# Kernel tuning notes

Measured on AMD Instinct MI355X. Metric: run time of the kernel, lower is better.

## Reference

```python
import jax, jax.numpy as jnp
from jax import lax
import numpy as np

N_NEURON = 4096
BATCH = 64
N_STEP = 200


def setup_inputs() -> dict:
    key = jax.random.key(0)
    k1, k2, k3 = jax.random.split(key, 3)
    # state_g is a sigmoid output: keep strictly inside (0, 1) for g_inverse's log
    state_g = jax.random.uniform(k1, (BATCH, N_NEURON), dtype=jnp.float32,
                                 minval=0.05, maxval=0.95)
    # Symmetric_Linear init: W ~ N(0, 0.01), symmetrized, zero diagonal
    W = jax.random.normal(k2, (N_NEURON, N_NEURON), dtype=jnp.float32) * 0.01
    W = W + W.T
    W = W - jnp.diag(jnp.diag(W))
    b = jax.random.normal(k3, (N_NEURON,), dtype=jnp.float32) * 0.01
    beta = jnp.ones((N_NEURON,), dtype=jnp.float32) * 10.0
    tau = jnp.ones((N_NEURON,), dtype=jnp.float32)
    dt_train = jnp.float32(0.1)
    return {"state_g": state_g, "W": W, "b": b, "beta": beta, "tau": tau,
            "dt_train": dt_train, "n_step": N_STEP}


def reference(state_g, W, b, beta, tau, dt_train, n_step):
    # max_x = 50 / beta.max()  (original uses .item(); beta is constant so same value)
    max_x = 50.0 / jnp.max(beta)
    # Symmetric_Linear effective weight: (W + W^T)/2 with zero diagonal.
    # Original recomputes this every step; it's step-invariant so hoist it.
    W_sym = (W + W.T) * 0.5 - jnp.diag(jnp.diag(W))
    # g_inverse: x = (1/beta) * log(g / (1 - g))
    state_x = (1.0 / beta) * jnp.log(state_g / (1.0 - state_g))
    alpha = dt_train / tau  # [N]

    def step(carry, _):
        x, g = carry
        pre = g @ W_sym.T + b                       # [B, N] GEMM
        x = alpha * pre + (1.0 - alpha) * x         # leaky update
        x = jnp.clip(x, -max_x, max_x)
        g = jax.nn.sigmoid(beta * x)
        return (x, g), None

    (state_x, state_g), _ = lax.scan(step, (state_x, state_g), None, length=n_step)
    return state_g
```

## Files before the change

kernel.cpp:

```cpp
#include <hip/hip_runtime.h>
#include <hip/hip_bf16.h>

#define MM 64
#define NN 4096
#define KK 4096
#define NSTEP 200
#define NSLICE 8
#define NSTRIP 32
#define NPART 8

typedef __bf16 bf16x8 __attribute__((ext_vector_type(8)));
typedef float  f32x4  __attribute__((ext_vector_type(4)));

static __device__ __forceinline__ unsigned short f2bf(float f) {
    __hip_bfloat16 h = __float2bfloat16(f);
    return __builtin_bit_cast(unsigned short, h);
}
static __device__ __forceinline__ float bf2f(unsigned short u) {
    __hip_bfloat16 h = __builtin_bit_cast(__hip_bfloat16, u);
    return __bfloat162float(h);
}


__global__ __launch_bounds__(256) void symm_kernel(const float* __restrict__ W,
                                                   unsigned short* __restrict__ Wfh,
                                                   unsigned short* __restrict__ Wfl) {
    __shared__ float T[64][65];
    const int tid = threadIdx.x;
    const int r0 = blockIdx.y * 64, c0 = blockIdx.x * 64;
#pragma unroll
    for (int i = 0; i < 4; ++i) {
        int lin = tid + i * 256;
        int cc  = lin >> 4;
        int r4  = (lin & 15) * 4;
        float4 v = *(const float4*)&W[(size_t)(c0 + cc) * NN + r0 + r4];
        T[cc][r4 + 0] = v.x; T[cc][r4 + 1] = v.y;
        T[cc][r4 + 2] = v.z; T[cc][r4 + 3] = v.w;
    }
    __syncthreads();
#pragma unroll
    for (int i = 0; i < 4; ++i) {
        int lin = tid + i * 256;
        int rr  = lin >> 4;
        int c4  = (lin & 15) * 4;
        float4 v = *(const float4*)&W[(size_t)(r0 + rr) * NN + c0 + c4];
        float d[4] = {v.x, v.y, v.z, v.w};
        ushort4 ohi, olo;
        unsigned short* ph = (unsigned short*)&ohi;
        unsigned short* pl = (unsigned short*)&olo;
#pragma unroll
        for (int j = 0; j < 4; ++j) {
            float sv = 0.5f * (d[j] + T[c4 + j][rr]);
            if (r0 + rr == c0 + c4 + j) sv = 0.0f;
            unsigned short hi = f2bf(sv);
            ph[j] = hi;
            pl[j] = f2bf(sv - bf2f(hi));
        }
        const int n  = r0 + rr;
        const int kg = c0 + c4;
        const int s_ = n >> 7, ns = (n >> 4) & 7, ln = n & 15;
        const int kc = kg >> 5, q = (kg & 31) >> 3, j0 = kg & 7;
        size_t off = ((((size_t)(s_ * 8 + ns) * 128 + kc) * 64 + q * 16 + ln)) * 8 + j0;
        *(ushort4*)&Wfh[off] = ohi;
        *(ushort4*)&Wfl[off] = olo;
    }
}

__global__ __launch_bounds__(256) void init_kernel(const float* __restrict__ g_in,
                                                   const float* __restrict__ beta,
                                                   float* __restrict__ x,
                                                   unsigned short* __restrict__ gfh,
                                                   unsigned short* __restrict__ gfl) {
    int idx = blockIdx.x * 256 + threadIdx.x;
    int r = idx >> 12, c = idx & (NN - 1);
    float g = g_in[idx];
    x[idx] = logf(g / (1.0f - g)) / beta[c];
    unsigned short hi = f2bf(g);
    unsigned short lo = f2bf(g - bf2f(hi));
    size_t off = (((size_t)(c >> 5) * 4 + (r >> 4)) * 64 + ((c & 31) >> 3) * 16 + (r & 15)) * 8 + (c & 7);
    gfh[off] = hi;
    gfl[off] = lo;
}

__global__ __launch_bounds__(256) void maxx_kernel(const float* __restrict__ beta,
                                                   float* __restrict__ out) {
    __shared__ float red[256];
    float m = -1e30f;
    for (int i = threadIdx.x; i < NN; i += 256) m = fmaxf(m, beta[i]);
    red[threadIdx.x] = m;
    __syncthreads();
    for (int s = 128; s > 0; s >>= 1) {
        if (threadIdx.x < s) red[threadIdx.x] = fmaxf(red[threadIdx.x], red[threadIdx.x + s]);
        __syncthreads();
    }
    if (threadIdx.x == 0) out[0] = 50.0f / red[0];
}

__global__ __launch_bounds__(1024, 1) void gemm_kernel(
    const unsigned short* __restrict__ gfh,
    const unsigned short* __restrict__ gfl,
    const unsigned short* __restrict__ Wfh,
    const unsigned short* __restrict__ Wfl,
    float* __restrict__ P)
{
    __shared__ float sacc[12][32][64];

    const int tid  = threadIdx.x;
    const int w    = tid >> 6;
    const int lane = tid & 63;
    const int q    = lane >> 4;
    const int l16  = lane & 15;

    const int s = blockIdx.x >> 3;
    const int k = blockIdx.x & 7;

    const int mh = w & 1;
    const int nh = (w >> 1) & 1;
    const int kh = w >> 2;

    f32x4 acc[2][4] = {};

#pragma unroll
    for (int it = 0; it < 4; ++it) {
        const int kc = k * 16 + kh * 4 + it;
        const size_t aBase = ((size_t)kc * 4) * 512 + lane * 8;
        const size_t bBase = (((size_t)(s * 8) * 128 + kc) * 64 + lane) * 8;
        bf16x8 ah[2], al[2], bh[4], bl[4];
#pragma unroll
        for (int mi = 0; mi < 2; ++mi) {
            const size_t a = aBase + (size_t)(mh * 2 + mi) * 512;
            ah[mi] = *(const bf16x8*)&gfh[a];
            al[mi] = *(const bf16x8*)&gfl[a];
        }
#pragma unroll
        for (int ni = 0; ni < 4; ++ni) {
            const size_t b = bBase + (size_t)(nh * 4 + ni) * 128 * 512;
            bh[ni] = *(const bf16x8*)&Wfh[b];
            bl[ni] = *(const bf16x8*)&Wfl[b];
        }
#pragma unroll
        for (int mi = 0; mi < 2; ++mi)
#pragma unroll
            for (int ni = 0; ni < 4; ++ni) {
                acc[mi][ni] = __builtin_amdgcn_mfma_f32_16x16x32_bf16(ah[mi], bh[ni], acc[mi][ni], 0, 0, 0);
                acc[mi][ni] = __builtin_amdgcn_mfma_f32_16x16x32_bf16(al[mi], bh[ni], acc[mi][ni], 0, 0, 0);
                acc[mi][ni] = __builtin_amdgcn_mfma_f32_16x16x32_bf16(ah[mi], bl[ni], acc[mi][ni], 0, 0, 0);
            }
    }

    if (kh > 0) {
#pragma unroll
        for (int mi = 0; mi < 2; ++mi)
#pragma unroll
            for (int ni = 0; ni < 4; ++ni)
#pragma unroll
                for (int rg = 0; rg < 4; ++rg)
                    sacc[w - 4][(mi * 4 + ni) * 4 + rg][lane] = acc[mi][ni][rg];
    }
    __syncthreads();
    if (kh == 0) {
        float* Pb = &P[((size_t)(k * NSTRIP + s) * 64) * 128];
#pragma unroll
        for (int mi = 0; mi < 2; ++mi)
#pragma unroll
            for (int ni = 0; ni < 4; ++ni)
#pragma unroll
                for (int rg = 0; rg < 4; ++rg) {
                    const int idx = (mi * 4 + ni) * 4 + rg;
                    const int row = mh * 32 + mi * 16 + q * 4 + rg;
                    const int col = nh * 64 + ni * 16 + l16;
                    float v = acc[mi][ni][rg]
                            + sacc[w][idx][lane]
                            + sacc[w + 4][idx][lane]
                            + sacc[w + 8][idx][lane];
                    Pb[(size_t)row * 128 + col] = v;
                }
    }
}

__global__ __launch_bounds__(256) void epi_kernel(
    const float* __restrict__ P,
    float* __restrict__ x,
    unsigned short* __restrict__ gfh_out,
    unsigned short* __restrict__ gfl_out,
    const float* __restrict__ bvec,
    const float* __restrict__ beta,
    const float* __restrict__ tau,
    const float* __restrict__ dt_ptr,
    const float* __restrict__ maxx_ptr,
    float* __restrict__ gout_f32)
{
    const int t  = blockIdx.x * 256 + threadIdx.x;
    const int m  = t >> 9;
    const int n0 = (t & 511) * 8;
    const int s  = n0 >> 7;

    float sum[8] = {};
#pragma unroll
    for (int k = 0; k < NPART; ++k) {
        const float* p = &P[((size_t)(k * NSTRIP + s) * 64 + m) * 128 + (n0 & 127)];
        float4 p0 = *(const float4*)&p[0];
        float4 p1 = *(const float4*)&p[4];
        sum[0] += p0.x; sum[1] += p0.y; sum[2] += p0.z; sum[3] += p0.w;
        sum[4] += p1.x; sum[5] += p1.y; sum[6] += p1.z; sum[7] += p1.w;
    }

    const float dt = *dt_ptr;
    const float mx = *maxx_ptr;
    float4 b0 = *(const float4*)&bvec[n0], b1 = *(const float4*)&bvec[n0 + 4];
    float4 e0 = *(const float4*)&beta[n0], e1 = *(const float4*)&beta[n0 + 4];
    float4 t0 = *(const float4*)&tau[n0],  t1 = *(const float4*)&tau[n0 + 4];
    float bb[8] = {b0.x, b0.y, b0.z, b0.w, b1.x, b1.y, b1.z, b1.w};
    float be[8] = {e0.x, e0.y, e0.z, e0.w, e1.x, e1.y, e1.z, e1.w};
    float tv[8] = {t0.x, t0.y, t0.z, t0.w, t1.x, t1.y, t1.z, t1.w};

    float* xp = &x[(size_t)m * NN + n0];
    float4 x0 = *(const float4*)&xp[0], x1 = *(const float4*)&xp[4];
    float xo[8] = {x0.x, x0.y, x0.z, x0.w, x1.x, x1.y, x1.z, x1.w};

    float gg[8];
    unsigned short vh[8], vl[8];
#pragma unroll
    for (int j = 0; j < 8; ++j) {
        const float al = dt / tv[j];
        float xn = al * (sum[j] + bb[j]) + (1.0f - al) * xo[j];
        xn = fminf(fmaxf(xn, -mx), mx);
        float g = 1.0f / (1.0f + __expf(-be[j] * xn));
        xo[j] = xn;
        gg[j] = g;
        unsigned short hi = f2bf(g);
        vh[j] = hi;
        vl[j] = f2bf(g - bf2f(hi));
    }
    *(float4*)&xp[0] = {xo[0], xo[1], xo[2], xo[3]};
    *(float4*)&xp[4] = {xo[4], xo[5], xo[6], xo[7]};

    size_t off = (((size_t)(n0 >> 5) * 4 + (m >> 4)) * 64 + ((n0 & 31) >> 3) * 16 + (m & 15)) * 8;
    *(ushort4*)&gfh_out[off]     = {vh[0], vh[1], vh[2], vh[3]};
    *(ushort4*)&gfh_out[off + 4] = {vh[4], vh[5], vh[6], vh[7]};
    *(ushort4*)&gfl_out[off]     = {vl[0], vl[1], vl[2], vl[3]};
    *(ushort4*)&gfl_out[off + 4] = {vl[4], vl[5], vl[6], vl[7]};

    if (gout_f32) {
        *(float4*)&gout_f32[(size_t)m * NN + n0]     = {gg[0], gg[1], gg[2], gg[3]};
        *(float4*)&gout_f32[(size_t)m * NN + n0 + 4] = {gg[4], gg[5], gg[6], gg[7]};
    }
}

extern "C" void kernel_launch(void* const* d_in, const int* in_sizes, int n_in,
                              void* d_out, int out_size, void* d_ws, size_t ws_size,
                              hipStream_t stream) {
    const float* state_g = (const float*)d_in[0];
    const float* W       = (const float*)d_in[1];
    const float* b       = (const float*)d_in[2];
    const float* beta    = (const float*)d_in[3];
    const float* tau     = (const float*)d_in[4];
    const float* dt      = (const float*)d_in[5];
    float* out = (float*)d_out;

    char* ws = (char*)d_ws;
    const size_t WH = (size_t)KK * NN * 2;
    const size_t XB = (size_t)MM * NN * 4;
    const size_t GB = (size_t)MM * NN * 2;
    const size_t PB = (size_t)NPART * NSTRIP * 64 * 128 * 4;
    unsigned short* Wfh = (unsigned short*)ws;
    unsigned short* Wfl = (unsigned short*)(ws + WH);
    float*          x   = (float*)(ws + 2 * WH);
    unsigned short* g0h = (unsigned short*)(ws + 2 * WH + XB);
    unsigned short* g0l = (unsigned short*)(ws + 2 * WH + XB + GB);
    unsigned short* g1h = (unsigned short*)(ws + 2 * WH + XB + 2 * GB);
    unsigned short* g1l = (unsigned short*)(ws + 2 * WH + XB + 3 * GB);
    float*          P   = (float*)(ws + 2 * WH + XB + 4 * GB);
    float*          mxp = (float*)(ws + 2 * WH + XB + 4 * GB + PB);

    symm_kernel<<<dim3(64, 64), 256, 0, stream>>>(W, Wfh, Wfl);
    init_kernel<<<(MM * NN) / 256, 256, 0, stream>>>(state_g, beta, x, g0h, g0l);
    maxx_kernel<<<1, 256, 0, stream>>>(beta, mxp);

    unsigned short *gih = g0h, *gil = g0l, *goh = g1h, *gol = g1l;
    for (int st = 0; st < NSTEP; ++st) {
        float* of = (st == NSTEP - 1) ? out : nullptr;
        gemm_kernel<<<NSTRIP * NSLICE, 1024, 0, stream>>>(gih, gil, Wfh, Wfl, P);
        epi_kernel<<<128, 256, 0, stream>>>(P, x, goh, gol, b, beta, tau, dt, mxp, of);
        unsigned short* tp;
        tp = gih; gih = goh; goh = tp;
        tp = gil; gil = gol; gol = tp;
    }
}
```

Before: 3.831 ms.

## Switch split-precision GEMM to fp16 hi/lo plus scaled fp8 W residual

Replaces the bf16 hi/lo three-MFMA emulation of the fp32 GEMM with fp16 hi/lo for activations and an fp8 residual of W, scaled by 16384, computed in a separate fp8 MFMA accumulator. W's low part shrinks from 2 bytes to 1 byte per element, which reduces the per-step weight stream that dominates memory traffic, and fp16 gives more mantissa bits for the high part. It also remaps the gemm block order (k-major) and changes the epilogue to 256 blocks of 128 threads. The risks are fp16 range and fp8 precision loss in the correction term, plus extra fp8 activation buffers that must be written every step.

```diff
diff --git a/kernel.cpp b/kernel.cpp
--- a/kernel.cpp
+++ b/kernel.cpp
@@ -9,22 +9,24 @@
 #define NSTRIP 32
 #define NPART 8
 
-typedef __bf16 bf16x8 __attribute__((ext_vector_type(8)));
-typedef float  f32x4  __attribute__((ext_vector_type(4)));
-
-static __device__ __forceinline__ unsigned short f2bf(float f) {
-    __hip_bfloat16 h = __float2bfloat16(f);
+#define WLO_SCALE 16384.0f
+#define WLO_INV   6.103515625e-05f
+
+typedef _Float16 f16x8 __attribute__((ext_vector_type(8)));
+typedef float    f32x4 __attribute__((ext_vector_type(4)));
+
+static __device__ __forceinline__ unsigned short f2h(float f) {
+    _Float16 h = (_Float16)f;
     return __builtin_bit_cast(unsigned short, h);
 }
-static __device__ __forceinline__ float bf2f(unsigned short u) {
-    __hip_bfloat16 h = __builtin_bit_cast(__hip_bfloat16, u);
-    return __bfloat162float(h);
+static __device__ __forceinline__ float h2f(unsigned short u) {
+    return (float)__builtin_bit_cast(_Float16, u);
 }
 
 
 __global__ __launch_bounds__(256) void symm_kernel(const float* __restrict__ W,
                                                    unsigned short* __restrict__ Wfh,
-                                                   unsigned short* __restrict__ Wfl) {
+                                                   unsigned char*  __restrict__ Wfl8) {
     __shared__ float T[64][65];
     const int tid = threadIdx.x;
     const int r0 = blockIdx.y * 64, c0 = blockIdx.x * 64;
@@ -45,24 +47,27 @@
         int c4  = (lin & 15) * 4;
         float4 v = *(const float4*)&W[(size_t)(r0 + rr) * NN + c0 + c4];
         float d[4] = {v.x, v.y, v.z, v.w};
-        ushort4 ohi, olo;
+        ushort4 ohi;
         unsigned short* ph = (unsigned short*)&ohi;
-        unsigned short* pl = (unsigned short*)&olo;
+        float rs[4];
 #pragma unroll
         for (int j = 0; j < 4; ++j) {
             float sv = 0.5f * (d[j] + T[c4 + j][rr]);
             if (r0 + rr == c0 + c4 + j) sv = 0.0f;
-            unsigned short hi = f2bf(sv);
+            unsigned short hi = f2h(sv);
             ph[j] = hi;
-            pl[j] = f2bf(sv - bf2f(hi));
+            rs[j] = (sv - h2f(hi)) * WLO_SCALE;
         }
+        int pk = __builtin_amdgcn_cvt_pk_fp8_f32(rs[0], rs[1], 0, false);
+        pk     = __builtin_amdgcn_cvt_pk_fp8_f32(rs[2], rs[3], pk, true);
+
         const int n  = r0 + rr;
         const int kg = c0 + c4;
         const int s_ = n >> 7, ns = (n >> 4) & 7, ln = n & 15;
         const int kc = kg >> 5, q = (kg & 31) >> 3, j0 = kg & 7;
         size_t off = ((((size_t)(s_ * 8 + ns) * 128 + kc) * 64 + q * 16 + ln)) * 8 + j0;
         *(ushort4*)&Wfh[off] = ohi;
-        *(ushort4*)&Wfl[off] = olo;
+        *(unsigned int*)&Wfl8[off] = (unsigned int)pk;
     }
 }
 
@@ -70,16 +75,18 @@
                                                    const float* __restrict__ beta,
                                                    float* __restrict__ x,
                                                    unsigned short* __restrict__ gfh,
-                                                   unsigned short* __restrict__ gfl) {
+                                                   unsigned short* __restrict__ gfl,
+                                                   unsigned char*  __restrict__ gf8) {
     int idx = blockIdx.x * 256 + threadIdx.x;
     int r = idx >> 12, c = idx & (NN - 1);
     float g = g_in[idx];
     x[idx] = logf(g / (1.0f - g)) / beta[c];
-    unsigned short hi = f2bf(g);
-    unsigned short lo = f2bf(g - bf2f(hi));
+    unsigned short hi = f2h(g);
     size_t off = (((size_t)(c >> 5) * 4 + (r >> 4)) * 64 + ((c & 31) >> 3) * 16 + (r & 15)) * 8 + (c & 7);
     gfh[off] = hi;
-    gfl[off] = lo;
+    gfl[off] = f2h(g - h2f(hi));
+    int p8 = __builtin_amdgcn_cvt_pk_fp8_f32(g, g, 0, false);
+    gf8[off] = (unsigned char)(p8 & 0xff);
 }
 
 __global__ __launch_bounds__(256) void maxx_kernel(const float* __restrict__ beta,
@@ -99,8 +106,9 @@
 __global__ __launch_bounds__(1024, 1) void gemm_kernel(
     const unsigned short* __restrict__ gfh,
     const unsigned short* __restrict__ gfl,
+    const unsigned char*  __restrict__ gf8,
     const unsigned short* __restrict__ Wfh,
-    const unsigned short* __restrict__ Wfl,
+    const unsigned char*  __restrict__ Wfl8,
     float* __restrict__ P)
 {
     __shared__ float sacc[12][32][64];
@@ -111,43 +119,56 @@
     const int q    = lane >> 4;
     const int l16  = lane & 15;
 
-    const int s = blockIdx.x >> 3;
-    const int k = blockIdx.x & 7;
+    const int k = blockIdx.x >> 5;
+    const int s = blockIdx.x & 31;
 
     const int mh = w & 1;
     const int nh = (w >> 1) & 1;
     const int kh = w >> 2;
 
-    f32x4 acc[2][4] = {};
+    f32x4 acc[2][4]  = {};
+    f32x4 acc8[2][4] = {};
 
 #pragma unroll
     for (int it = 0; it < 4; ++it) {
         const int kc = k * 16 + kh * 4 + it;
-        const size_t aBase = ((size_t)kc * 4) * 512 + lane * 8;
-        const size_t bBase = (((size_t)(s * 8) * 128 + kc) * 64 + lane) * 8;
-        bf16x8 ah[2], al[2], bh[4], bl[4];
+        const size_t aB = ((size_t)kc * 4) * 512 + lane * 8;
+        const size_t bB = (((size_t)(s * 8) * 128 + kc) * 64 + lane) * 8;
+        f16x8 ah[2], al[2], bh[4];
+        unsigned long long a8[2], b8[4];
 #pragma unroll
         for (int mi = 0; mi < 2; ++mi) {
-            const size_t a = aBase + (size_t)(mh * 2 + mi) * 512;
-            ah[mi] = *(const bf16x8*)&gfh[a];
-            al[mi] = *(const bf16x8*)&gfl[a];
+            const size_t a = aB + (size_t)(mh * 2 + mi) * 512;
+            ah[mi] = *(const f16x8*)&gfh[a];
+            al[mi] = *(const f16x8*)&gfl[a];
+            a8[mi] = *(const unsigned long long*)&gf8[a];
         }
 #pragma unroll
         for (int ni = 0; ni < 4; ++ni) {
-            const size_t b = bBase + (size_t)(nh * 4 + ni) * 128 * 512;
-            bh[ni] = *(const bf16x8*)&Wfh[b];
-            bl[ni] = *(const bf16x8*)&Wfl[b];
+            const size_t b = bB + (size_t)(nh * 4 + ni) * 128 * 512;
+            bh[ni] = *(const f16x8*)&Wfh[b];
+            b8[ni] = *(const unsigned long long*)&Wfl8[b];
         }
 #pragma unroll
         for (int mi = 0; mi < 2; ++mi)
 #pragma unroll
             for (int ni = 0; ni < 4; ++ni) {
-                acc[mi][ni] = __builtin_amdgcn_mfma_f32_16x16x32_bf16(ah[mi], bh[ni], acc[mi][ni], 0, 0, 0);
-                acc[mi][ni] = __builtin_amdgcn_mfma_f32_16x16x32_bf16(al[mi], bh[ni], acc[mi][ni], 0, 0, 0);
-                acc[mi][ni] = __builtin_amdgcn_mfma_f32_16x16x32_bf16(ah[mi], bl[ni], acc[mi][ni], 0, 0, 0);
+                acc[mi][ni]  = __builtin_amdgcn_mfma_f32_16x16x32_f16(ah[mi], bh[ni], acc[mi][ni], 0, 0, 0);
+                acc[mi][ni]  = __builtin_amdgcn_mfma_f32_16x16x32_f16(al[mi], bh[ni], acc[mi][ni], 0, 0, 0);
+                acc8[mi][ni] = __builtin_amdgcn_mfma_f32_16x16x32_fp8_fp8(
+                                   (long long)a8[mi], (long long)b8[ni], acc8[mi][ni], 0, 0, 0);
             }
     }
 
+    float t[2][4][4];
+#pragma unroll
+    for (int mi = 0; mi < 2; ++mi)
+#pragma unroll
+        for (int ni = 0; ni < 4; ++ni)
+#pragma unroll
+            for (int rg = 0; rg < 4; ++rg)
+                t[mi][ni][rg] = acc[mi][ni][rg] + acc8[mi][ni][rg] * WLO_INV;
+
     if (kh > 0) {
 #pragma unroll
         for (int mi = 0; mi < 2; ++mi)
@@ -155,7 +176,7 @@
             for (int ni = 0; ni < 4; ++ni)
 #pragma unroll
                 for (int rg = 0; rg < 4; ++rg)
-                    sacc[w - 4][(mi * 4 + ni) * 4 + rg][lane] = acc[mi][ni][rg];
+                    sacc[w - 4][(mi * 4 + ni) * 4 + rg][lane] = t[mi][ni][rg];
     }
     __syncthreads();
     if (kh == 0) {
@@ -169,7 +190,7 @@
                     const int idx = (mi * 4 + ni) * 4 + rg;
                     const int row = mh * 32 + mi * 16 + q * 4 + rg;
                     const int col = nh * 64 + ni * 16 + l16;
-                    float v = acc[mi][ni][rg]
+                    float v = t[mi][ni][rg]
                             + sacc[w][idx][lane]
                             + sacc[w + 4][idx][lane]
                             + sacc[w + 8][idx][lane];
@@ -178,11 +199,12 @@
     }
 }
 
-__global__ __launch_bounds__(256) void epi_kernel(
+__global__ __launch_bounds__(128) void epi_kernel(
     const float* __restrict__ P,
     float* __restrict__ x,
     unsigned short* __restrict__ gfh_out,
     unsigned short* __restrict__ gfl_out,
+    unsigned char*  __restrict__ gf8_out,
     const float* __restrict__ bvec,
     const float* __restrict__ beta,
     const float* __restrict__ tau,
@@ -190,15 +212,15 @@
     const float* __restrict__ maxx_ptr,
     float* __restrict__ gout_f32)
 {
-    const int t  = blockIdx.x * 256 + threadIdx.x;
-    const int m  = t >> 9;
-    const int n0 = (t & 511) * 8;
-    const int s  = n0 >> 7;
+    const int tid = threadIdx.x;
+    const int s   = blockIdx.x & 31;
+    const int m   = (blockIdx.x >> 5) * 8 + (tid >> 4);
+    const int n0  = s * 128 + (tid & 15) * 8;
 
     float sum[8] = {};
 #pragma unroll
-    for (int k = 0; k < NPART; ++k) {
-        const float* p = &P[((size_t)(k * NSTRIP + s) * 64 + m) * 128 + (n0 & 127)];
+    for (int kp = 0; kp < NPART; ++kp) {
+        const float* p = &P[((size_t)(kp * NSTRIP + s) * 64 + m) * 128 + (n0 & 127)];
         float4 p0 = *(const float4*)&p[0];
         float4 p1 = *(const float4*)&p[4];
         sum[0] += p0.x; sum[1] += p0.y; sum[2] += p0.z; sum[3] += p0.w;
@@ -228,9 +250,9 @@
         float g = 1.0f / (1.0f + __expf(-be[j] * xn));
         xo[j] = xn;
         gg[j] = g;
-        unsigned short hi = f2bf(g);
+        unsigned short hi = f2h(g);
         vh[j] = hi;
-        vl[j] = f2bf(g - bf2f(hi));
+        vl[j] = f2h(g - h2f(hi));
     }
     *(float4*)&xp[0] = {xo[0], xo[1], xo[2], xo[3]};
     *(float4*)&xp[4] = {xo[4], xo[5], xo[6], xo[7]};
@@ -240,6 +262,13 @@
     *(ushort4*)&gfh_out[off + 4] = {vh[4], vh[5], vh[6], vh[7]};
     *(ushort4*)&gfl_out[off]     = {vl[0], vl[1], vl[2], vl[3]};
     *(ushort4*)&gfl_out[off + 4] = {vl[4], vl[5], vl[6], vl[7]};
+
+    int p0i = __builtin_amdgcn_cvt_pk_fp8_f32(gg[0], gg[1], 0, false);
+    p0i     = __builtin_amdgcn_cvt_pk_fp8_f32(gg[2], gg[3], p0i, true);
+    int p1i = __builtin_amdgcn_cvt_pk_fp8_f32(gg[4], gg[5], 0, false);
+    p1i     = __builtin_amdgcn_cvt_pk_fp8_f32(gg[6], gg[7], p1i, true);
+    *(unsigned int*)&gf8_out[off]     = (unsigned int)p0i;
+    *(unsigned int*)&gf8_out[off + 4] = (unsigned int)p1i;
 
     if (gout_f32) {
         *(float4*)&gout_f32[(size_t)m * NN + n0]     = {gg[0], gg[1], gg[2], gg[3]};
@@ -260,30 +289,38 @@
 
     char* ws = (char*)d_ws;
     const size_t WH = (size_t)KK * NN * 2;
+    const size_t WL = (size_t)KK * NN;
     const size_t XB = (size_t)MM * NN * 4;
-    const size_t GB = (size_t)MM * NN * 2;
+    const size_t GH = (size_t)MM * NN * 2;
+    const size_t G8 = (size_t)MM * NN;
     const size_t PB = (size_t)NPART * NSTRIP * 64 * 128 * 4;
-    unsigned short* Wfh = (unsigned short*)ws;
-    unsigned short* Wfl = (unsigned short*)(ws + WH);
-    float*          x   = (float*)(ws + 2 * WH);
-    unsigned short* g0h = (unsigned short*)(ws + 2 * WH + XB);
-    unsigned short* g0l = (unsigned short*)(ws + 2 * WH + XB + GB);
-    unsigned short* g1h = (unsigned short*)(ws + 2 * WH + XB + 2 * GB);
-    unsigned short* g1l = (unsigned short*)(ws + 2 * WH + XB + 3 * GB);
-    float*          P   = (float*)(ws + 2 * WH + XB + 4 * GB);
-    float*          mxp = (float*)(ws + 2 * WH + XB + 4 * GB + PB);
-
-    symm_kernel<<<dim3(64, 64), 256, 0, stream>>>(W, Wfh, Wfl);
-    init_kernel<<<(MM * NN) / 256, 256, 0, stream>>>(state_g, beta, x, g0h, g0l);
+
+    unsigned short* Wfh  = (unsigned short*)ws;
+    unsigned char*  Wfl8 = (unsigned char*)(ws + WH);
+    float*          x    = (float*)(ws + WH + WL);
+    char* gbase = ws + WH + WL + XB;
+    unsigned short* g0h = (unsigned short*)(gbase);
+    unsigned short* g0l = (unsigned short*)(gbase + GH);
+    unsigned char*  g08 = (unsigned char*)(gbase + 2 * GH);
+    unsigned short* g1h = (unsigned short*)(gbase + 2 * GH + G8);
+    unsigned short* g1l = (unsigned short*)(gbase + 3 * GH + G8);
+    unsigned char*  g18 = (unsigned char*)(gbase + 4 * GH + G8);
+    float*          P   = (float*)(gbase + 4 * GH + 2 * G8);
+    float*          mxp = (float*)(gbase + 4 * GH + 2 * G8 + PB);
+
+    symm_kernel<<<dim3(64, 64), 256, 0, stream>>>(W, Wfh, Wfl8);
+    init_kernel<<<(MM * NN) / 256, 256, 0, stream>>>(state_g, beta, x, g0h, g0l, g08);
     maxx_kernel<<<1, 256, 0, stream>>>(beta, mxp);
 
     unsigned short *gih = g0h, *gil = g0l, *goh = g1h, *gol = g1l;
+    unsigned char  *gi8 = g08, *go8 = g18;
     for (int st = 0; st < NSTEP; ++st) {
         float* of = (st == NSTEP - 1) ? out : nullptr;
-        gemm_kernel<<<NSTRIP * NSLICE, 1024, 0, stream>>>(gih, gil, Wfh, Wfl, P);
-        epi_kernel<<<128, 256, 0, stream>>>(P, x, goh, gol, b, beta, tau, dt, mxp, of);
+        gemm_kernel<<<NSTRIP * NSLICE, 1024, 0, stream>>>(gih, gil, gi8, Wfh, Wfl8, P);
+        epi_kernel<<<256, 128, 0, stream>>>(P, x, goh, gol, go8, b, beta, tau, dt, mxp, of);
         unsigned short* tp;
         tp = gih; gih = goh; goh = tp;
         tp = gil; gil = gol; gol = tp;
-    }
-}
+        unsigned char* t8 = gi8; gi8 = go8; go8 = t8;
+    }
+}
```

New measurement: 4.022 ms. +5.0%, slower.

## Double split-K slices and shrink per-block tile to raise GEMM occupancy

Applied to the files above, without the earlier changes.

The GEMM grid grows from 256 to 512 blocks by splitting K into 16 slices instead of 8. Each block now does two K-halves of four chunks, with waves covering a 2x4 M/N quadrant grid, so the in-block reduction needs only one LDS partial. Shared memory shrinks, the launch-bounds hint now allows more resident blocks, and block index order changes so consecutive blocks share a K slice. The cost is twice as many partial tiles written to P and read back by the epilogue, which is remapped to 256 blocks of 128 threads.

```diff
diff --git a/kernel.cpp b/kernel.cpp
--- a/kernel.cpp
+++ b/kernel.cpp
@@ -5,9 +5,9 @@
 #define NN 4096
 #define KK 4096
 #define NSTEP 200
-#define NSLICE 8
+#define NSLICE 16
 #define NSTRIP 32
-#define NPART 8
+#define NPART 16
 
 typedef __bf16 bf16x8 __attribute__((ext_vector_type(8)));
 typedef float  f32x4  __attribute__((ext_vector_type(4)));
@@ -96,14 +96,14 @@
     if (threadIdx.x == 0) out[0] = 50.0f / red[0];
 }
 
-__global__ __launch_bounds__(1024, 1) void gemm_kernel(
+__global__ __launch_bounds__(1024, 8) void gemm_kernel(
     const unsigned short* __restrict__ gfh,
     const unsigned short* __restrict__ gfl,
     const unsigned short* __restrict__ Wfh,
     const unsigned short* __restrict__ Wfl,
     float* __restrict__ P)
 {
-    __shared__ float sacc[12][32][64];
+    __shared__ float sacc[8][16][64];
 
     const int tid  = threadIdx.x;
     const int w    = tid >> 6;
@@ -111,51 +111,51 @@
     const int q    = lane >> 4;
     const int l16  = lane & 15;
 
-    const int s = blockIdx.x >> 3;
-    const int k = blockIdx.x & 7;
+    const int k = blockIdx.x >> 5;
+    const int s = blockIdx.x & 31;
 
     const int mh = w & 1;
-    const int nh = (w >> 1) & 1;
-    const int kh = w >> 2;
-
-    f32x4 acc[2][4] = {};
+    const int nq = (w >> 1) & 3;
+    const int kh = w >> 3;
+
+    f32x4 acc[2][2] = {};
 
 #pragma unroll
     for (int it = 0; it < 4; ++it) {
-        const int kc = k * 16 + kh * 4 + it;
-        const size_t aBase = ((size_t)kc * 4) * 512 + lane * 8;
-        const size_t bBase = (((size_t)(s * 8) * 128 + kc) * 64 + lane) * 8;
-        bf16x8 ah[2], al[2], bh[4], bl[4];
+        const int kc = k * 8 + kh * 4 + it;
+        const size_t aB = ((size_t)kc * 4) * 512 + lane * 8;
+        const size_t bB = (((size_t)(s * 8) * 128 + kc) * 64 + lane) * 8;
+        bf16x8 ah[2], al[2], bh[2], bl[2];
 #pragma unroll
         for (int mi = 0; mi < 2; ++mi) {
-            const size_t a = aBase + (size_t)(mh * 2 + mi) * 512;
+            const size_t a = aB + (size_t)(mh * 2 + mi) * 512;
             ah[mi] = *(const bf16x8*)&gfh[a];
             al[mi] = *(const bf16x8*)&gfl[a];
         }
 #pragma unroll
-        for (int ni = 0; ni < 4; ++ni) {
-            const size_t b = bBase + (size_t)(nh * 4 + ni) * 128 * 512;
+        for (int ni = 0; ni < 2; ++ni) {
+            const size_t b = bB + (size_t)(nq * 2 + ni) * 128 * 512;
             bh[ni] = *(const bf16x8*)&Wfh[b];
             bl[ni] = *(const bf16x8*)&Wfl[b];
         }
 #pragma unroll
         for (int mi = 0; mi < 2; ++mi)
 #pragma unroll
-            for (int ni = 0; ni < 4; ++ni) {
+            for (int ni = 0; ni < 2; ++ni) {
                 acc[mi][ni] = __builtin_amdgcn_mfma_f32_16x16x32_bf16(ah[mi], bh[ni], acc[mi][ni], 0, 0, 0);
                 acc[mi][ni] = __builtin_amdgcn_mfma_f32_16x16x32_bf16(al[mi], bh[ni], acc[mi][ni], 0, 0, 0);
                 acc[mi][ni] = __builtin_amdgcn_mfma_f32_16x16x32_bf16(ah[mi], bl[ni], acc[mi][ni], 0, 0, 0);
             }
     }
 
-    if (kh > 0) {
+    if (kh == 1) {
 #pragma unroll
         for (int mi = 0; mi < 2; ++mi)
 #pragma unroll
-            for (int ni = 0; ni < 4; ++ni)
+            for (int ni = 0; ni < 2; ++ni)
 #pragma unroll
                 for (int rg = 0; rg < 4; ++rg)
-                    sacc[w - 4][(mi * 4 + ni) * 4 + rg][lane] = acc[mi][ni][rg];
+                    sacc[w - 8][(mi * 2 + ni) * 4 + rg][lane] = acc[mi][ni][rg];
     }
     __syncthreads();
     if (kh == 0) {
@@ -163,22 +163,18 @@
 #pragma unroll
         for (int mi = 0; mi < 2; ++mi)
 #pragma unroll
-            for (int ni = 0; ni < 4; ++ni)
+            for (int ni = 0; ni < 2; ++ni)
 #pragma unroll
                 for (int rg = 0; rg < 4; ++rg) {
-                    const int idx = (mi * 4 + ni) * 4 + rg;
+                    const int idx = (mi * 2 + ni) * 4 + rg;
                     const int row = mh * 32 + mi * 16 + q * 4 + rg;
-                    const int col = nh * 64 + ni * 16 + l16;
-                    float v = acc[mi][ni][rg]
-                            + sacc[w][idx][lane]
-                            + sacc[w + 4][idx][lane]
-                            + sacc[w + 8][idx][lane];
-                    Pb[(size_t)row * 128 + col] = v;
+                    const int col = nq * 32 + ni * 16 + l16;
+                    Pb[(size_t)row * 128 + col] = acc[mi][ni][rg] + sacc[w][idx][lane];
                 }
     }
 }
 
-__global__ __launch_bounds__(256) void epi_kernel(
+__global__ __launch_bounds__(128) void epi_kernel(
     const float* __restrict__ P,
     float* __restrict__ x,
     unsigned short* __restrict__ gfh_out,
@@ -190,15 +186,15 @@
     const float* __restrict__ maxx_ptr,
     float* __restrict__ gout_f32)
 {
-    const int t  = blockIdx.x * 256 + threadIdx.x;
-    const int m  = t >> 9;
-    const int n0 = (t & 511) * 8;
-    const int s  = n0 >> 7;
+    const int tid = threadIdx.x;
+    const int s   = blockIdx.x & 31;
+    const int m   = (blockIdx.x >> 5) * 8 + (tid >> 4);
+    const int n0  = s * 128 + (tid & 15) * 8;
 
     float sum[8] = {};
 #pragma unroll
-    for (int k = 0; k < NPART; ++k) {
-        const float* p = &P[((size_t)(k * NSTRIP + s) * 64 + m) * 128 + (n0 & 127)];
+    for (int kp = 0; kp < NPART; ++kp) {
+        const float* p = &P[((size_t)(kp * NSTRIP + s) * 64 + m) * 128 + (n0 & 127)];
         float4 p0 = *(const float4*)&p[0];
         float4 p1 = *(const float4*)&p[4];
         sum[0] += p0.x; sum[1] += p0.y; sum[2] += p0.z; sum[3] += p0.w;
@@ -281,7 +277,7 @@
     for (int st = 0; st < NSTEP; ++st) {
         float* of = (st == NSTEP - 1) ? out : nullptr;
         gemm_kernel<<<NSTRIP * NSLICE, 1024, 0, stream>>>(gih, gil, Wfh, Wfl, P);
-        epi_kernel<<<128, 256, 0, stream>>>(P, x, goh, gol, b, beta, tau, dt, mxp, of);
+        epi_kernel<<<256, 128, 0, stream>>>(P, x, goh, gol, b, beta, tau, dt, mxp, of);
         unsigned short* tp;
         tp = gih; gih = goh; goh = tp;
         tp = gil; gil = gol; gol = tp;
```

New measurement: 4.353 ms. 13.6% more time.
